# Performance work log

Measured on AMD Instinct MI355X. Metric: run time of the kernel, lower is better.

## Reference

```python
import jax, jax.numpy as jnp
import numpy as np

B, T, I, H, O = 64, 2048, 128, 256, 128

def setup_inputs() -> dict:
    key = jax.random.key(0)
    ks = jax.random.split(key, 7)
    return {
        "x": jax.random.normal(ks[0], (B, T, I), dtype=jnp.float32),
        "Wi": jax.random.normal(ks[1], (H, I), dtype=jnp.float32) / np.sqrt(I),
        "bi": jax.random.normal(ks[2], (H,), dtype=jnp.float32) * 0.01,
        "Wh": jax.random.normal(ks[3], (H, H), dtype=jnp.float32) / np.sqrt(H),
        "bh": jax.random.normal(ks[4], (H,), dtype=jnp.float32) * 0.01,
        "Wo": jax.random.normal(ks[5], (O, H), dtype=jnp.float32) / np.sqrt(H),
        "bo": jax.random.normal(ks[6], (O,), dtype=jnp.float32) * 0.01,
    }

def reference(x, Wi, bi, Wh, bh, Wo, bo):
    # x: [B, T, I]; torch Linear weights are [out, in] -> right-multiply by W.T
    b = x.shape[0]
    h0 = jnp.zeros((b, Wh.shape[0]), dtype=x.dtype)
    # precompute input projection for all timesteps (batched GEMM)
    xproj = jnp.einsum('bti,hi->bth', x, Wi) + bi  # [B, T, H]

    def step(h, xp_t):
        h = jnp.tanh(xp_t + h @ Wh.T + bh)
        return h, h

    _, hs = jax.lax.scan(step, h0, jnp.swapaxes(xproj, 0, 1))  # hs: [T, B, H]
    hs = jnp.swapaxes(hs, 0, 1)  # [B, T, H]
    out = jnp.einsum('bth,oh->bto', hs, Wo) + bo  # [B, T, O]
    return out
```

## Files before the change

### kernel.cpp

```cpp
#include <hip/hip_runtime.h>
#include <hip/hip_bf16.h>

#define BB 64
#define TT 2048
#define II 128
#define HH 256
#define OO 128

typedef float f32x4v __attribute__((ext_vector_type(4)));
typedef short bf16x8 __attribute__((ext_vector_type(8)));
typedef unsigned short ushortv4 __attribute__((ext_vector_type(4)));

__device__ __forceinline__ float bf16bits_to_f32(unsigned short u) {
    return __uint_as_float((unsigned)u << 16);
}
__device__ __forceinline__ unsigned short f2bf(float f) {
    union { __hip_bfloat16 h; unsigned short u; } cv;
    cv.h = __float2bfloat16(f);
    return cv.u;
}
__device__ __forceinline__ float tanh_fast(float x) {
    float y = x * 2.88539008177793f;
    float e;
    asm("v_exp_f32 %0, %1" : "=v"(e) : "v"(y));
    return 1.0f - 2.0f * __builtin_amdgcn_rcpf(e + 1.0f);
}


#define BM 64
#define BN 64
#define BKT 32

__global__ __launch_bounds__(256) void gemm_f32_bt(
    const float* __restrict__ A, const float* __restrict__ B,
    const float* __restrict__ bias, const float* __restrict__ bias2,
    float* __restrict__ C, int M, int N, int K)
{
    __shared__ __align__(16) float As[BKT][BM + 4];
    __shared__ __align__(16) float Bs[BKT][BN + 4];

    const int t  = threadIdx.x;
    const int m0 = blockIdx.x * BM;
    const int n0 = blockIdx.y * BN;
    const int r  = t >> 3;
    const int kq = (t & 7) * 4;
    const int tx = t & 15;
    const int ty = t >> 4;

    float acc[4][4] = {};

    for (int k0 = 0; k0 < K; k0 += BKT) {
        float4 a0 = *(const float4*)&A[(size_t)(m0 + r)      * K + k0 + kq];
        float4 a1 = *(const float4*)&A[(size_t)(m0 + r + 32) * K + k0 + kq];
        float4 b0 = *(const float4*)&B[(size_t)(n0 + r)      * K + k0 + kq];
        float4 b1 = *(const float4*)&B[(size_t)(n0 + r + 32) * K + k0 + kq];

        __syncthreads();
        As[kq + 0][r] = a0.x; As[kq + 1][r] = a0.y; As[kq + 2][r] = a0.z; As[kq + 3][r] = a0.w;
        As[kq + 0][r + 32] = a1.x; As[kq + 1][r + 32] = a1.y; As[kq + 2][r + 32] = a1.z; As[kq + 3][r + 32] = a1.w;
        Bs[kq + 0][r] = b0.x; Bs[kq + 1][r] = b0.y; Bs[kq + 2][r] = b0.z; Bs[kq + 3][r] = b0.w;
        Bs[kq + 0][r + 32] = b1.x; Bs[kq + 1][r + 32] = b1.y; Bs[kq + 2][r + 32] = b1.z; Bs[kq + 3][r + 32] = b1.w;
        __syncthreads();

#pragma unroll
        for (int k = 0; k < BKT; ++k) {
            float4 avv = *(const float4*)&As[k][ty * 4];
            float4 bvv = *(const float4*)&Bs[k][tx * 4];
            const float* av = &avv.x;
            const float* bv = &bvv.x;
#pragma unroll
            for (int i = 0; i < 4; ++i)
#pragma unroll
                for (int j = 0; j < 4; ++j)
                    acc[i][j] = fmaf(av[i], bv[j], acc[i][j]);
        }
    }

#pragma unroll
    for (int i = 0; i < 4; ++i) {
#pragma unroll
        for (int j = 0; j < 4; ++j) {
            const int c = n0 + tx * 4 + j;
            float v = acc[i][j] + bias[c] + bias2[c];
            const int pos = (c & ~31) + 2 * (c & 15) + ((c & 31) >> 4);
            C[(size_t)(m0 + ty * 4 + i) * N + pos] = v;
        }
    }
}

__global__ __launch_bounds__(256) void gemm_bf16a_bt(
    const unsigned short* __restrict__ A, const float* __restrict__ B,
    const float* __restrict__ bias, float* __restrict__ C,
    int M, int N, int K)
{
    __shared__ __align__(16) float As[BKT][BM + 4];
    __shared__ __align__(16) float Bs[BKT][BN + 4];

    const int t  = threadIdx.x;
    const int m0 = blockIdx.x * BM;
    const int n0 = blockIdx.y * BN;
    const int r  = t >> 3;
    const int kq = (t & 7) * 4;
    const int kh = kq >> 1;
    const int tx = t & 15;
    const int ty = t >> 4;

    float acc[4][4] = {};

    for (int k0 = 0; k0 < K; k0 += BKT) {
        ushortv4 a0 = *(const ushortv4*)&A[(size_t)(m0 + r)      * K + k0 + kq];
        ushortv4 a1 = *(const ushortv4*)&A[(size_t)(m0 + r + 32) * K + k0 + kq];
        float4  b0 = *(const float4*)&B[(size_t)(n0 + r)      * K + k0 + kq];
        float4  b1 = *(const float4*)&B[(size_t)(n0 + r + 32) * K + k0 + kq];

        __syncthreads();
        As[kh + 0][r]  = bf16bits_to_f32(a0[0]); As[kh + 16][r] = bf16bits_to_f32(a0[1]);
        As[kh + 1][r]  = bf16bits_to_f32(a0[2]); As[kh + 17][r] = bf16bits_to_f32(a0[3]);
        As[kh + 0][r + 32]  = bf16bits_to_f32(a1[0]); As[kh + 16][r + 32] = bf16bits_to_f32(a1[1]);
        As[kh + 1][r + 32]  = bf16bits_to_f32(a1[2]); As[kh + 17][r + 32] = bf16bits_to_f32(a1[3]);
        Bs[kq + 0][r] = b0.x; Bs[kq + 1][r] = b0.y; Bs[kq + 2][r] = b0.z; Bs[kq + 3][r] = b0.w;
        Bs[kq + 0][r + 32] = b1.x; Bs[kq + 1][r + 32] = b1.y; Bs[kq + 2][r + 32] = b1.z; Bs[kq + 3][r + 32] = b1.w;
        __syncthreads();

#pragma unroll
        for (int k = 0; k < BKT; ++k) {
            float4 avv = *(const float4*)&As[k][ty * 4];
            float4 bvv = *(const float4*)&Bs[k][tx * 4];
            const float* av = &avv.x;
            const float* bv = &bvv.x;
#pragma unroll
            for (int i = 0; i < 4; ++i)
#pragma unroll
                for (int j = 0; j < 4; ++j)
                    acc[i][j] = fmaf(av[i], bv[j], acc[i][j]);
        }
    }

#pragma unroll
    for (int i = 0; i < 4; ++i) {
        float4 o;
        o.x = acc[i][0] + bias[n0 + tx * 4 + 0];
        o.y = acc[i][1] + bias[n0 + tx * 4 + 1];
        o.z = acc[i][2] + bias[n0 + tx * 4 + 2];
        o.w = acc[i][3] + bias[n0 + tx * 4 + 3];
        *(float4*)&C[(size_t)(m0 + ty * 4 + i) * N + n0 + tx * 4] = o;
    }
}

#define G 16
#define HPAD 264

__global__ __launch_bounds__(512) __attribute__((amdgpu_waves_per_eu(2, 2)))
void rnn_recurrence_mfma(
    const float* __restrict__ xproj, const float* __restrict__ Wh,
    unsigned short* __restrict__ hs)
{
    __shared__ __align__(16) unsigned short hbl[2][G][HPAD];

    const int blk  = blockIdx.x;
    const int tid  = threadIdx.x;
    const int wave = tid >> 6;
    const int lane = tid & 63;
    const int l15  = lane & 15;
    const int lg   = lane >> 4;
    const int n0   = wave * 32;

#define LOADB(nt, kt, dst) { \
        const float* wp = Wh + (size_t)(n0 + (nt)*16 + l15) * HH + (kt)*32 + lg*4; \
        dst[0] = (short)f2bf(wp[0]);  dst[1] = (short)f2bf(wp[16]); \
        dst[2] = (short)f2bf(wp[1]);  dst[3] = (short)f2bf(wp[17]); \
        dst[4] = (short)f2bf(wp[2]);  dst[5] = (short)f2bf(wp[18]); \
        dst[6] = (short)f2bf(wp[3]);  dst[7] = (short)f2bf(wp[19]); }

    bf16x8 B00, B01, B02, B03, B04, B05, B06, B07;
    bf16x8 B10, B11, B12, B13, B14, B15, B16, B17;
    LOADB(0, 0, B00) LOADB(0, 1, B01) LOADB(0, 2, B02) LOADB(0, 3, B03)
    LOADB(0, 4, B04) LOADB(0, 5, B05) LOADB(0, 6, B06) LOADB(0, 7, B07)
    LOADB(1, 0, B10) LOADB(1, 1, B11) LOADB(1, 2, B12) LOADB(1, 3, B13)
    LOADB(1, 4, B14) LOADB(1, 5, B15) LOADB(1, 6, B16) LOADB(1, 7, B17)

    const int mb = blk * G + lg * 4;
    const float* xq0 = xproj + (size_t)(mb + 0) * TT * HH + n0 + 2 * l15;
    const float* xq1 = xproj + (size_t)(mb + 1) * TT * HH + n0 + 2 * l15;
    const float* xq2 = xproj + (size_t)(mb + 2) * TT * HH + n0 + 2 * l15;
    const float* xq3 = xproj + (size_t)(mb + 3) * TT * HH + n0 + 2 * l15;
    unsigned short* hq0 = hs + (size_t)(mb + 0) * TT * HH + n0 + 2 * l15;
    unsigned short* hq1 = hs + (size_t)(mb + 1) * TT * HH + n0 + 2 * l15;
    unsigned short* hq2 = hs + (size_t)(mb + 2) * TT * HH + n0 + 2 * l15;
    unsigned short* hq3 = hs + (size_t)(mb + 3) * TT * HH + n0 + 2 * l15;

    for (int i = tid; i < G * HPAD / 2; i += 512)
        ((unsigned int*)hbl[0])[i] = 0u;
    float2 xv0 = *(const float2*)xq0;
    float2 xv1 = *(const float2*)xq1;
    float2 xv2 = *(const float2*)xq2;
    float2 xv3 = *(const float2*)xq3;
    __syncthreads();

    unsigned int sv0 = 0, sv1 = 0, sv2 = 0, sv3 = 0;

    for (int t = 0; t < TT; ++t) {
        const int p = t & 1;

        const unsigned short* hrow = &hbl[p][l15][lg * 8];
        bf16x8 a0 = *(const bf16x8*)(hrow + 0 * 32);
        bf16x8 a1 = *(const bf16x8*)(hrow + 1 * 32);
        bf16x8 a2 = *(const bf16x8*)(hrow + 2 * 32);
        bf16x8 a3 = *(const bf16x8*)(hrow + 3 * 32);
        bf16x8 a4 = *(const bf16x8*)(hrow + 4 * 32);
        bf16x8 a5 = *(const bf16x8*)(hrow + 5 * 32);
        bf16x8 a6 = *(const bf16x8*)(hrow + 6 * 32);
        bf16x8 a7 = *(const bf16x8*)(hrow + 7 * 32);

        if (t) {
            *(unsigned int*)hq0 = sv0; hq0 += HH;
            *(unsigned int*)hq1 = sv1; hq1 += HH;
            *(unsigned int*)hq2 = sv2; hq2 += HH;
            *(unsigned int*)hq3 = sv3; hq3 += HH;
        }

        f32x4v c0 = {xv0.x, xv1.x, xv2.x, xv3.x};
        f32x4v c1 = {xv0.y, xv1.y, xv2.y, xv3.y};
        c0 = __builtin_amdgcn_mfma_f32_16x16x32_bf16(a0, B00, c0, 0, 0, 0);
        c1 = __builtin_amdgcn_mfma_f32_16x16x32_bf16(a0, B10, c1, 0, 0, 0);
        c0 = __builtin_amdgcn_mfma_f32_16x16x32_bf16(a1, B01, c0, 0, 0, 0);
        c1 = __builtin_amdgcn_mfma_f32_16x16x32_bf16(a1, B11, c1, 0, 0, 0);
        c0 = __builtin_amdgcn_mfma_f32_16x16x32_bf16(a2, B02, c0, 0, 0, 0);
        c1 = __builtin_amdgcn_mfma_f32_16x16x32_bf16(a2, B12, c1, 0, 0, 0);
        c0 = __builtin_amdgcn_mfma_f32_16x16x32_bf16(a3, B03, c0, 0, 0, 0);
        c1 = __builtin_amdgcn_mfma_f32_16x16x32_bf16(a3, B13, c1, 0, 0, 0);
        c0 = __builtin_amdgcn_mfma_f32_16x16x32_bf16(a4, B04, c0, 0, 0, 0);
        c1 = __builtin_amdgcn_mfma_f32_16x16x32_bf16(a4, B14, c1, 0, 0, 0);
        c0 = __builtin_amdgcn_mfma_f32_16x16x32_bf16(a5, B05, c0, 0, 0, 0);
        c1 = __builtin_amdgcn_mfma_f32_16x16x32_bf16(a5, B15, c1, 0, 0, 0);
        c0 = __builtin_amdgcn_mfma_f32_16x16x32_bf16(a6, B06, c0, 0, 0, 0);
        c1 = __builtin_amdgcn_mfma_f32_16x16x32_bf16(a6, B16, c1, 0, 0, 0);
        c0 = __builtin_amdgcn_mfma_f32_16x16x32_bf16(a7, B07, c0, 0, 0, 0);
        c1 = __builtin_amdgcn_mfma_f32_16x16x32_bf16(a7, B17, c1, 0, 0, 0);

#define EPI(r, sv) { \
        float h0 = tanh_fast(c0[r]); \
        float h1 = tanh_fast(c1[r]); \
        asm("v_cvt_pk_bf16_f32 %0, %1, %2" : "=v"(sv) : "v"(h0), "v"(h1)); \
        *(unsigned int*)&hbl[p ^ 1][lg * 4 + (r)][n0 + 2 * l15] = sv; }

        EPI(0, sv0)
        EPI(1, sv1)
        EPI(2, sv2)
        EPI(3, sv3)

        xq0 += HH; xq1 += HH; xq2 += HH; xq3 += HH;
        xv0 = *(const float2*)xq0;
        xv1 = *(const float2*)xq1;
        xv2 = *(const float2*)xq2;
        xv3 = *(const float2*)xq3;

        __syncthreads();
    }

    *(unsigned int*)hq0 = sv0;
    *(unsigned int*)hq1 = sv1;
    *(unsigned int*)hq2 = sv2;
    *(unsigned int*)hq3 = sv3;
}

extern "C" void kernel_launch(void* const* d_in, const int* in_sizes, int n_in,
                              void* d_out, int out_size, void* d_ws, size_t ws_size,
                              hipStream_t stream)
{
    const float* x  = (const float*)d_in[0];
    const float* Wi = (const float*)d_in[1];
    const float* bi = (const float*)d_in[2];
    const float* Wh = (const float*)d_in[3];
    const float* bh = (const float*)d_in[4];
    const float* Wo = (const float*)d_in[5];
    const float* bo = (const float*)d_in[6];
    float* out = (float*)d_out;

    const int M = BB * TT;

    float* xproj = (float*)d_ws;
    unsigned short* hs = (unsigned short*)((char*)d_ws + (size_t)M * HH * sizeof(float));

    gemm_f32_bt<<<dim3(M / BM, HH / BN), 256, 0, stream>>>(x, Wi, bi, bh, xproj, M, HH, II);

    rnn_recurrence_mfma<<<dim3(4), 512, 0, stream>>>(xproj, Wh, hs);

    gemm_bf16a_bt<<<dim3(M / BM, OO / BN), 256, 0, stream>>>(
        hs, Wo, bo, out, M, OO, HH);
}
```

Before: 1.410 ms.

## Replace FP32 SIMT projection GEMMs with bf16 MFMA kernels

The input-projection and output-projection GEMMs move from scalar FP32 FMA tiling kernels to bf16 MFMA kernels. Each block stages the whole weight matrix in LDS as bf16, and each wave computes a 16-row strip across all output columns. The output GEMM folds the permuted hidden-column order into the LDS weight layout. This cuts the compute cost of the two large GEMMs, but x is now rounded to bf16, which lowers input-projection precision, and every block reconverts the full weight matrix.

```diff
diff --git a/kernel.cpp b/kernel.cpp
--- a/kernel.cpp
+++ b/kernel.cpp
@@ -9,11 +9,7 @@
 
 typedef float f32x4v __attribute__((ext_vector_type(4)));
 typedef short bf16x8 __attribute__((ext_vector_type(8)));
-typedef unsigned short ushortv4 __attribute__((ext_vector_type(4)));
-
-__device__ __forceinline__ float bf16bits_to_f32(unsigned short u) {
-    return __uint_as_float((unsigned)u << 16);
-}
+
 __device__ __forceinline__ unsigned short f2bf(float f) {
     union { __hip_bfloat16 h; unsigned short u; } cv;
     cv.h = __float2bfloat16(f);
@@ -27,123 +23,105 @@
 }
 
 
-#define BM 64
-#define BN 64
-#define BKT 32
-
-__global__ __launch_bounds__(256) void gemm_f32_bt(
-    const float* __restrict__ A, const float* __restrict__ B,
-    const float* __restrict__ bias, const float* __restrict__ bias2,
-    float* __restrict__ C, int M, int N, int K)
-{
-    __shared__ __align__(16) float As[BKT][BM + 4];
-    __shared__ __align__(16) float Bs[BKT][BN + 4];
-
-    const int t  = threadIdx.x;
-    const int m0 = blockIdx.x * BM;
-    const int n0 = blockIdx.y * BN;
-    const int r  = t >> 3;
-    const int kq = (t & 7) * 4;
-    const int tx = t & 15;
-    const int ty = t >> 4;
-
-    float acc[4][4] = {};
-
-    for (int k0 = 0; k0 < K; k0 += BKT) {
-        float4 a0 = *(const float4*)&A[(size_t)(m0 + r)      * K + k0 + kq];
-        float4 a1 = *(const float4*)&A[(size_t)(m0 + r + 32) * K + k0 + kq];
-        float4 b0 = *(const float4*)&B[(size_t)(n0 + r)      * K + k0 + kq];
-        float4 b1 = *(const float4*)&B[(size_t)(n0 + r + 32) * K + k0 + kq];
-
-        __syncthreads();
-        As[kq + 0][r] = a0.x; As[kq + 1][r] = a0.y; As[kq + 2][r] = a0.z; As[kq + 3][r] = a0.w;
-        As[kq + 0][r + 32] = a1.x; As[kq + 1][r + 32] = a1.y; As[kq + 2][r + 32] = a1.z; As[kq + 3][r + 32] = a1.w;
-        Bs[kq + 0][r] = b0.x; Bs[kq + 1][r] = b0.y; Bs[kq + 2][r] = b0.z; Bs[kq + 3][r] = b0.w;
-        Bs[kq + 0][r + 32] = b1.x; Bs[kq + 1][r + 32] = b1.y; Bs[kq + 2][r + 32] = b1.z; Bs[kq + 3][r + 32] = b1.w;
-        __syncthreads();
-
-#pragma unroll
-        for (int k = 0; k < BKT; ++k) {
-            float4 avv = *(const float4*)&As[k][ty * 4];
-            float4 bvv = *(const float4*)&Bs[k][tx * 4];
-            const float* av = &avv.x;
-            const float* bv = &bvv.x;
-#pragma unroll
-            for (int i = 0; i < 4; ++i)
-#pragma unroll
-                for (int j = 0; j < 4; ++j)
-                    acc[i][j] = fmaf(av[i], bv[j], acc[i][j]);
-        }
-    }
-
-#pragma unroll
-    for (int i = 0; i < 4; ++i) {
-#pragma unroll
-        for (int j = 0; j < 4; ++j) {
-            const int c = n0 + tx * 4 + j;
-            float v = acc[i][j] + bias[c] + bias2[c];
-            const int pos = (c & ~31) + 2 * (c & 15) + ((c & 31) >> 4);
-            C[(size_t)(m0 + ty * 4 + i) * N + pos] = v;
-        }
-    }
-}
-
-__global__ __launch_bounds__(256) void gemm_bf16a_bt(
-    const unsigned short* __restrict__ A, const float* __restrict__ B,
-    const float* __restrict__ bias, float* __restrict__ C,
-    int M, int N, int K)
-{
-    __shared__ __align__(16) float As[BKT][BM + 4];
-    __shared__ __align__(16) float Bs[BKT][BN + 4];
-
-    const int t  = threadIdx.x;
-    const int m0 = blockIdx.x * BM;
-    const int n0 = blockIdx.y * BN;
-    const int r  = t >> 3;
-    const int kq = (t & 7) * 4;
-    const int kh = kq >> 1;
-    const int tx = t & 15;
-    const int ty = t >> 4;
-
-    float acc[4][4] = {};
-
-    for (int k0 = 0; k0 < K; k0 += BKT) {
-        ushortv4 a0 = *(const ushortv4*)&A[(size_t)(m0 + r)      * K + k0 + kq];
-        ushortv4 a1 = *(const ushortv4*)&A[(size_t)(m0 + r + 32) * K + k0 + kq];
-        float4  b0 = *(const float4*)&B[(size_t)(n0 + r)      * K + k0 + kq];
-        float4  b1 = *(const float4*)&B[(size_t)(n0 + r + 32) * K + k0 + kq];
-
-        __syncthreads();
-        As[kh + 0][r]  = bf16bits_to_f32(a0[0]); As[kh + 16][r] = bf16bits_to_f32(a0[1]);
-        As[kh + 1][r]  = bf16bits_to_f32(a0[2]); As[kh + 17][r] = bf16bits_to_f32(a0[3]);
-        As[kh + 0][r + 32]  = bf16bits_to_f32(a1[0]); As[kh + 16][r + 32] = bf16bits_to_f32(a1[1]);
-        As[kh + 1][r + 32]  = bf16bits_to_f32(a1[2]); As[kh + 17][r + 32] = bf16bits_to_f32(a1[3]);
-        Bs[kq + 0][r] = b0.x; Bs[kq + 1][r] = b0.y; Bs[kq + 2][r] = b0.z; Bs[kq + 3][r] = b0.w;
-        Bs[kq + 0][r + 32] = b1.x; Bs[kq + 1][r + 32] = b1.y; Bs[kq + 2][r + 32] = b1.z; Bs[kq + 3][r + 32] = b1.w;
-        __syncthreads();
-
-#pragma unroll
-        for (int k = 0; k < BKT; ++k) {
-            float4 avv = *(const float4*)&As[k][ty * 4];
-            float4 bvv = *(const float4*)&Bs[k][tx * 4];
-            const float* av = &avv.x;
-            const float* bv = &bvv.x;
-#pragma unroll
-            for (int i = 0; i < 4; ++i)
-#pragma unroll
-                for (int j = 0; j < 4; ++j)
-                    acc[i][j] = fmaf(av[i], bv[j], acc[i][j]);
-        }
-    }
-
-#pragma unroll
-    for (int i = 0; i < 4; ++i) {
-        float4 o;
-        o.x = acc[i][0] + bias[n0 + tx * 4 + 0];
-        o.y = acc[i][1] + bias[n0 + tx * 4 + 1];
-        o.z = acc[i][2] + bias[n0 + tx * 4 + 2];
-        o.w = acc[i][3] + bias[n0 + tx * 4 + 3];
-        *(float4*)&C[(size_t)(m0 + ty * 4 + i) * N + n0 + tx * 4] = o;
+#define MM(a, b, c) c = __builtin_amdgcn_mfma_f32_16x16x32_bf16(a, b, c, 0, 0, 0);
+
+#define WIPAD 136
+
+__global__ __launch_bounds__(256) void gemm1_mfma(
+    const float* __restrict__ x, const float* __restrict__ Wi,
+    const float* __restrict__ bi, const float* __restrict__ bh,
+    float* __restrict__ xproj)
+{
+    __shared__ __align__(16) unsigned short wiL[HH][WIPAD];
+
+    const int tid = threadIdx.x;
+    const int wv = tid >> 6, lane = tid & 63;
+    const int l15 = lane & 15, lg = lane >> 4;
+    const int m0 = blockIdx.x * 64 + wv * 16;
+
+    for (int e = tid; e < HH * II; e += 256)
+        wiL[e >> 7][e & 127] = f2bf(Wi[e]);
+    __syncthreads();
+
+    const float* xr = x + (size_t)(m0 + l15) * II + lg * 8;
+    bf16x8 a0, a1, a2, a3;
+#define LOADA1(q, dst) { \
+        float4 u0 = *(const float4*)(xr + (q) * 32); \
+        float4 u1 = *(const float4*)(xr + (q) * 32 + 4); \
+        dst[0] = (short)f2bf(u0.x); dst[1] = (short)f2bf(u0.y); \
+        dst[2] = (short)f2bf(u0.z); dst[3] = (short)f2bf(u0.w); \
+        dst[4] = (short)f2bf(u1.x); dst[5] = (short)f2bf(u1.y); \
+        dst[6] = (short)f2bf(u1.z); dst[7] = (short)f2bf(u1.w); }
+    LOADA1(0, a0) LOADA1(1, a1) LOADA1(2, a2) LOADA1(3, a3)
+
+#pragma unroll
+    for (int nt = 0; nt < 16; ++nt) {
+        const int c = nt * 16 + l15;
+        const float bv = bi[c] + bh[c];
+        f32x4v acc = {bv, bv, bv, bv};
+        const unsigned short* wrow = &wiL[nt * 16 + l15][lg * 8];
+        bf16x8 b0 = *(const bf16x8*)(wrow + 0);
+        bf16x8 b1 = *(const bf16x8*)(wrow + 32);
+        bf16x8 b2 = *(const bf16x8*)(wrow + 64);
+        bf16x8 b3 = *(const bf16x8*)(wrow + 96);
+        MM(a0, b0, acc) MM(a1, b1, acc) MM(a2, b2, acc) MM(a3, b3, acc)
+
+        const int pos = (c & ~31) + 2 * (c & 15) + ((c & 31) >> 4);
+#pragma unroll
+        for (int r = 0; r < 4; ++r)
+            xproj[(size_t)(m0 + lg * 4 + r) * HH + pos] = acc[r];
+    }
+}
+
+#define WOPAD 264
+
+__global__ __launch_bounds__(256) void gemm3_mfma(
+    const unsigned short* __restrict__ hs, const float* __restrict__ Wo,
+    const float* __restrict__ bo, float* __restrict__ out)
+{
+    __shared__ __align__(16) unsigned short woL[OO][WOPAD];
+
+    const int tid = threadIdx.x;
+    const int wv = tid >> 6, lane = tid & 63;
+    const int l15 = lane & 15, lg = lane >> 4;
+    const int m0 = blockIdx.x * 64 + wv * 16;
+
+    for (int e = tid; e < OO * HH; e += 256) {
+        const int o = e >> 8, c = e & 255;
+        const int pos = (c & ~31) + 2 * (c & 15) + ((c & 31) >> 4);
+        woL[o][pos] = f2bf(Wo[e]);
+    }
+    __syncthreads();
+
+    const unsigned short* hr = hs + (size_t)(m0 + l15) * HH + lg * 8;
+    bf16x8 a0 = *(const bf16x8*)(hr + 0);
+    bf16x8 a1 = *(const bf16x8*)(hr + 32);
+    bf16x8 a2 = *(const bf16x8*)(hr + 64);
+    bf16x8 a3 = *(const bf16x8*)(hr + 96);
+    bf16x8 a4 = *(const bf16x8*)(hr + 128);
+    bf16x8 a5 = *(const bf16x8*)(hr + 160);
+    bf16x8 a6 = *(const bf16x8*)(hr + 192);
+    bf16x8 a7 = *(const bf16x8*)(hr + 224);
+
+#pragma unroll
+    for (int nt = 0; nt < 8; ++nt) {
+        const float bv = bo[nt * 16 + l15];
+        f32x4v acc = {bv, bv, bv, bv};
+        const unsigned short* wrow = &woL[nt * 16 + l15][lg * 8];
+        bf16x8 b0 = *(const bf16x8*)(wrow + 0);
+        bf16x8 b1 = *(const bf16x8*)(wrow + 32);
+        bf16x8 b2 = *(const bf16x8*)(wrow + 64);
+        bf16x8 b3 = *(const bf16x8*)(wrow + 96);
+        bf16x8 b4 = *(const bf16x8*)(wrow + 128);
+        bf16x8 b5 = *(const bf16x8*)(wrow + 160);
+        bf16x8 b6 = *(const bf16x8*)(wrow + 192);
+        bf16x8 b7 = *(const bf16x8*)(wrow + 224);
+        MM(a0, b0, acc) MM(a1, b1, acc) MM(a2, b2, acc) MM(a3, b3, acc)
+        MM(a4, b4, acc) MM(a5, b5, acc) MM(a6, b6, acc) MM(a7, b7, acc)
+
+#pragma unroll
+        for (int r = 0; r < 4; ++r)
+            out[(size_t)(m0 + lg * 4 + r) * OO + nt * 16 + l15] = acc[r];
     }
 }
 
@@ -221,22 +199,14 @@
 
         f32x4v c0 = {xv0.x, xv1.x, xv2.x, xv3.x};
         f32x4v c1 = {xv0.y, xv1.y, xv2.y, xv3.y};
-        c0 = __builtin_amdgcn_mfma_f32_16x16x32_bf16(a0, B00, c0, 0, 0, 0);
-        c1 = __builtin_amdgcn_mfma_f32_16x16x32_bf16(a0, B10, c1, 0, 0, 0);
-        c0 = __builtin_amdgcn_mfma_f32_16x16x32_bf16(a1, B01, c0, 0, 0, 0);
-        c1 = __builtin_amdgcn_mfma_f32_16x16x32_bf16(a1, B11, c1, 0, 0, 0);
-        c0 = __builtin_amdgcn_mfma_f32_16x16x32_bf16(a2, B02, c0, 0, 0, 0);
-        c1 = __builtin_amdgcn_mfma_f32_16x16x32_bf16(a2, B12, c1, 0, 0, 0);
-        c0 = __builtin_amdgcn_mfma_f32_16x16x32_bf16(a3, B03, c0, 0, 0, 0);
-        c1 = __builtin_amdgcn_mfma_f32_16x16x32_bf16(a3, B13, c1, 0, 0, 0);
-        c0 = __builtin_amdgcn_mfma_f32_16x16x32_bf16(a4, B04, c0, 0, 0, 0);
-        c1 = __builtin_amdgcn_mfma_f32_16x16x32_bf16(a4, B14, c1, 0, 0, 0);
-        c0 = __builtin_amdgcn_mfma_f32_16x16x32_bf16(a5, B05, c0, 0, 0, 0);
-        c1 = __builtin_amdgcn_mfma_f32_16x16x32_bf16(a5, B15, c1, 0, 0, 0);
-        c0 = __builtin_amdgcn_mfma_f32_16x16x32_bf16(a6, B06, c0, 0, 0, 0);
-        c1 = __builtin_amdgcn_mfma_f32_16x16x32_bf16(a6, B16, c1, 0, 0, 0);
-        c0 = __builtin_amdgcn_mfma_f32_16x16x32_bf16(a7, B07, c0, 0, 0, 0);
-        c1 = __builtin_amdgcn_mfma_f32_16x16x32_bf16(a7, B17, c1, 0, 0, 0);
+        MM(a0, B00, c0) MM(a0, B10, c1)
+        MM(a1, B01, c0) MM(a1, B11, c1)
+        MM(a2, B02, c0) MM(a2, B12, c1)
+        MM(a3, B03, c0) MM(a3, B13, c1)
+        MM(a4, B04, c0) MM(a4, B14, c1)
+        MM(a5, B05, c0) MM(a5, B15, c1)
+        MM(a6, B06, c0) MM(a6, B16, c1)
+        MM(a7, B07, c0) MM(a7, B17, c1)
 
 #define EPI(r, sv) { \
         float h0 = tanh_fast(c0[r]); \
@@ -282,10 +252,9 @@
     float* xproj = (float*)d_ws;
     unsigned short* hs = (unsigned short*)((char*)d_ws + (size_t)M * HH * sizeof(float));
 
-    gemm_f32_bt<<<dim3(M / BM, HH / BN), 256, 0, stream>>>(x, Wi, bi, bh, xproj, M, HH, II);
+    gemm1_mfma<<<dim3(M / 64), 256, 0, stream>>>(x, Wi, bi, bh, xproj);
 
     rnn_recurrence_mfma<<<dim3(4), 512, 0, stream>>>(xproj, Wh, hs);
 
-    gemm_bf16a_bt<<<dim3(M / BM, OO / BN), 256, 0, stream>>>(
-        hs, Wo, bo, out, M, OO, HH);
-}
+    gemm3_mfma<<<dim3(M / 64), 256, 0, stream>>>(hs, Wo, bo, out);
+}
```

Result: faster. 1.263 ms (-10.4%).
